# Kernel optimization log

Measured on AMD Instinct MI355X. Metric: run time of the kernel, lower is better.

## Reference

```python
import jax, jax.numpy as jnp
import numpy as np


def setup_inputs() -> dict:
    key = jax.random.key(0)
    ks = jax.random.split(key, 9)
    B, Q, K, F, C = 16, 2048, 2048, 128, 2
    q = jax.random.normal(ks[0], (B, Q, F), dtype=jnp.float32)
    k = jax.random.normal(ks[1], (B, K, F), dtype=jnp.float32)
    v = jax.random.normal(ks[2], (B, K, F), dtype=jnp.float32)
    coords_q = jax.random.uniform(ks[3], (B, Q, C), dtype=jnp.float32)
    coords_k = jax.random.uniform(ks[4], (B, K, C), dtype=jnp.float32)
    attn_mask = jax.random.randint(ks[5], (B, Q, K), 0, 2).astype(jnp.bool_)
    alibi_mask = jax.random.randint(ks[6], (B, Q, K), 0, 2).astype(jnp.bool_)
    bias_scale = jax.random.uniform(ks[7], (1,), dtype=jnp.float32)  # nn.Parameter(torch.rand(1))
    running_mean = jnp.ones((1,), dtype=jnp.float32)  # RunningMeanScaler buffer (eval mode)
    return {"q": q, "k": k, "v": v, "coords_q": coords_q, "coords_k": coords_k,
            "attn_mask": attn_mask, "alibi_mask": alibi_mask,
            "bias_scale": bias_scale, "running_mean": running_mean}


def reference(q, k, v, coords_q, coords_k, attn_mask, alibi_mask, bias_scale, running_mean):
    # [b,q,k] attention logits
    scale = jnp.asarray(k.shape[-1], q.dtype) ** -0.5
    weight_logits = jnp.einsum('bqf,bkf->bqk', q, k) * scale
    # pairwise coordinate distances [b,q,k]
    diff = coords_q[:, :, None, :] - coords_k[:, None, :, :]
    distances = jnp.sqrt(jnp.sum(diff * diff, axis=-1))
    scaled_distances = (distances / running_mean) * bias_scale  # broadcast scalars
    masked_distances = jnp.where(alibi_mask, jnp.zeros((), distances.dtype), scaled_distances)
    weights = jax.nn.softmax(weight_logits, axis=-1)
    masked = jnp.where(attn_mask, jnp.zeros((), weights.dtype), weights - masked_distances)
    attention = jnp.einsum('bqk,bkf->bqf', masked, v)
    return attention
```

## Files before the change

### kernel.cpp

```cpp
#include <hip/hip_runtime.h>
#include <stdint.h>

#define B_  16
#define QL  2048
#define KL  2048
#define FD  128
#define BQ  64
#define BK  32

typedef __attribute__((ext_vector_type(8))) short bf16x8;
typedef __attribute__((ext_vector_type(4))) float f32x4;

__device__ __forceinline__ unsigned short f2b(float f) {
  union { float f; unsigned u; } x; x.f = f;
  unsigned r = x.u + 0x7fffu + ((x.u >> 16) & 1u);
  return (unsigned short)(r >> 16);
}

__global__ __launch_bounds__(256, 2) void alibi_attn(
    const float* __restrict__ qp,
    const float* __restrict__ kp,
    const float* __restrict__ vp,
    const float* __restrict__ cqp,
    const float* __restrict__ ckp,
    const int* __restrict__ amp,
    const int* __restrict__ almp,
    const float* __restrict__ bsp,
    const float* __restrict__ rmp,
    float* __restrict__ outp)
{
  __shared__ unsigned short kv[8192];
  __shared__ unsigned short plds[4][2][16 * 40];

  const int t    = threadIdx.x;
  const int w    = t >> 6;
  const int lane = t & 63;
  const int l15  = lane & 15;
  const int q4   = lane >> 4;

  const int bid  = blockIdx.x;
  const int xcd  = bid & 7, slot = bid >> 3;
  const int b    = (xcd << 1) | (slot >> 5);
  const int qt   = slot & 31;
  const int qbase = qt * BQ;

  const float bscale = bsp[0] / rmp[0];
  const float scale  = 0.08838834764831845f;

  {
    const float* qg = qp + ((long long)(b * QL + qbase)) * FD;
    #pragma unroll
    for (int i = 0; i < 8; ++i) {
      float4 u = ((const float4*)qg)[t + 256 * i];
      ushort4 s4;
      s4.x = f2b(u.x); s4.y = f2b(u.y); s4.z = f2b(u.z); s4.w = f2b(u.w);
      *(ushort4*)&kv[(t + 256 * i) * 4] = s4;
    }
  }
  __syncthreads();
  bf16x8 qfrag[4];
  {
    const int m = w * 16 + l15;
    #pragma unroll
    for (int fs = 0; fs < 4; ++fs)
      qfrag[fs] = *(const bf16x8*)&kv[m * 128 + fs * 32 + q4 * 8];
  }
  float cqx[4], cqy[4];
  #pragma unroll
  for (int r = 0; r < 4; ++r) {
    const int qg_ = qbase + w * 16 + q4 * 4 + r;
    cqx[r] = cqp[((long long)(b * QL + qg_)) * 2 + 0];
    cqy[r] = cqp[((long long)(b * QL + qg_)) * 2 + 1];
  }
  __syncthreads();

  f32x4 O1[8], O2[8];
  #pragma unroll
  for (int n = 0; n < 8; ++n) {
    O1[n] = (f32x4){0.f, 0.f, 0.f, 0.f};
    O2[n] = (f32x4){0.f, 0.f, 0.f, 0.f};
  }
  float lsum[4] = {0.f, 0.f, 0.f, 0.f};

  const int kr_st = t >> 3;
  const int fb_st = (t & 7) * 16;
  const float* kg_base = kp + ((long long)b * KL) * FD;
  const float* vg_base = vp + ((long long)b * KL) * FD;

  for (int kt = 0; kt < KL / BK; ++kt) {
    const int k0 = kt * BK;

    float4 kld[4], vld[4];
    #pragma unroll
    for (int i = 0; i < 4; ++i) {
      kld[i] = *(const float4*)(kg_base + (long long)(k0 + kr_st) * FD + fb_st + 4 * i);
      vld[i] = *(const float4*)(vg_base + (long long)(k0 + kr_st) * FD + fb_st + 4 * i);
    }
    int am_[2][4], al_[2][4];
    float ckx_[2], cky_[2];
    #pragma unroll
    for (int s = 0; s < 2; ++s) {
      const int kg = k0 + s * 16 + l15;
      #pragma unroll
      for (int r = 0; r < 4; ++r) {
        const int qg_ = qbase + w * 16 + q4 * 4 + r;
        const long long mi = ((long long)(b * QL + qg_)) * KL + kg;
        am_[s][r] = __builtin_nontemporal_load(amp + mi);
        al_[s][r] = __builtin_nontemporal_load(almp + mi);
      }
      float2 c2 = *(const float2*)(ckp + ((long long)(b * KL + kg)) * 2);
      ckx_[s] = c2.x; cky_[s] = c2.y;
    }

    __syncthreads();
    #pragma unroll
    for (int i = 0; i < 4; ++i) {
      ushort4 s4;
      s4.x = f2b(kld[i].x); s4.y = f2b(kld[i].y);
      s4.z = f2b(kld[i].z); s4.w = f2b(kld[i].w);
      *(ushort4*)&kv[kr_st * 128 + fb_st + 4 * i] = s4;
      const int f0 = fb_st + 4 * i;
      kv[4096 + (f0 + 0) * 32 + kr_st] = f2b(vld[i].x);
      kv[4096 + (f0 + 1) * 32 + kr_st] = f2b(vld[i].y);
      kv[4096 + (f0 + 2) * 32 + kr_st] = f2b(vld[i].z);
      kv[4096 + (f0 + 3) * 32 + kr_st] = f2b(vld[i].w);
    }
    __syncthreads();

    f32x4 S0 = (f32x4){0.f, 0.f, 0.f, 0.f};
    f32x4 S1 = (f32x4){0.f, 0.f, 0.f, 0.f};
    #pragma unroll
    for (int fs = 0; fs < 4; ++fs) {
      bf16x8 kb0 = *(const bf16x8*)&kv[(l15)      * 128 + fs * 32 + q4 * 8];
      bf16x8 kb1 = *(const bf16x8*)&kv[(16 + l15) * 128 + fs * 32 + q4 * 8];
      S0 = __builtin_amdgcn_mfma_f32_16x16x32_bf16(qfrag[fs], kb0, S0, 0, 0, 0);
      S1 = __builtin_amdgcn_mfma_f32_16x16x32_bf16(qfrag[fs], kb1, S1, 0, 0, 0);
    }

    #pragma unroll
    for (int s = 0; s < 2; ++s) {
      const f32x4 Sv = s ? S1 : S0;
      #pragma unroll
      for (int r = 0; r < 4; ++r) {
        float e = __expf(Sv[r] * scale);
        lsum[r] += e;
        float dx = cqx[r] - ckx_[s], dy = cqy[r] - cky_[s];
        float d  = sqrtf(fmaf(dx, dx, dy * dy)) * bscale;
        float wv = am_[s][r] ? 0.f : e;
        float tv = (am_[s][r] | al_[s][r]) ? 0.f : d;
        const int m = q4 * 4 + r, c = s * 16 + l15;
        plds[w][0][m * 40 + c] = f2b(wv);
        plds[w][1][m * 40 + c] = f2b(tv);
      }
    }
    __syncthreads();

    bf16x8 aw = *(const bf16x8*)&plds[w][0][l15 * 40 + q4 * 8];
    bf16x8 at = *(const bf16x8*)&plds[w][1][l15 * 40 + q4 * 8];
    #pragma unroll
    for (int n = 0; n < 8; ++n) {
      bf16x8 vb = *(const bf16x8*)&kv[4096 + (n * 16 + l15) * 32 + q4 * 8];
      O1[n] = __builtin_amdgcn_mfma_f32_16x16x32_bf16(aw, vb, O1[n], 0, 0, 0);
      O2[n] = __builtin_amdgcn_mfma_f32_16x16x32_bf16(at, vb, O2[n], 0, 0, 0);
    }
  }

  #pragma unroll
  for (int off = 1; off < 16; off <<= 1) {
    #pragma unroll
    for (int r = 0; r < 4; ++r) lsum[r] += __shfl_xor(lsum[r], off, 64);
  }
  float linv[4];
  #pragma unroll
  for (int r = 0; r < 4; ++r) linv[r] = 1.0f / lsum[r];

  #pragma unroll
  for (int n = 0; n < 8; ++n) {
    #pragma unroll
    for (int r = 0; r < 4; ++r) {
      const int qg_ = qbase + w * 16 + q4 * 4 + r;
      const int f   = n * 16 + l15;
      float val = O1[n][r] * linv[r] - O2[n][r];
      __builtin_nontemporal_store(val, outp + ((long long)(b * QL + qg_)) * FD + f);
    }
  }
}

extern "C" void kernel_launch(void* const* d_in, const int* in_sizes, int n_in,
                              void* d_out, int out_size, void* d_ws, size_t ws_size,
                              hipStream_t stream) {
  const float* q   = (const float*)d_in[0];
  const float* k   = (const float*)d_in[1];
  const float* v   = (const float*)d_in[2];
  const float* cq  = (const float*)d_in[3];
  const float* ck  = (const float*)d_in[4];
  const int*   am  = (const int*)d_in[5];
  const int*   alm = (const int*)d_in[6];
  const float* bs  = (const float*)d_in[7];
  const float* rm  = (const float*)d_in[8];
  float*       out = (float*)d_out;

  dim3 grid(B_ * (QL / BQ));
  dim3 block(256);
  hipLaunchKernelGGL(alibi_attn, grid, block, 0, stream,
                     q, k, v, cq, ck, am, alm, bs, rm, out);
}
```

Before: 751.9 us.

## Double-buffer K/V tiles in LDS with register prefetch and padded strides

Splits the K/V LDS staging into two buffers so the global loads (K, V, masks, coordinates) for the next tile are issued before the current tile's MFMAs, then converted and stored into the other buffer. This cuts the per-step barriers from three to one. It also pads the LDS row strides to reduce bank conflicts, switches exp to exp2 with a folded scale, and uses cheaper round-half-up bf16 conversion. The costs are doubled LDS and more registers, which may threaten two blocks per CU, plus slightly different rounding.

```diff
diff --git a/kernel.cpp b/kernel.cpp
--- a/kernel.cpp
+++ b/kernel.cpp
@@ -7,14 +7,20 @@
 #define FD  128
 #define BQ  64
 #define BK  32
+#define NSTEP (KL/BK)
+
+#define KSTR  136
+#define VTOFF 4352
+#define VTSTR 40
+#define BUFSHORTS 9472
+#define PSTR  40
 
 typedef __attribute__((ext_vector_type(8))) short bf16x8;
 typedef __attribute__((ext_vector_type(4))) float f32x4;
 
 __device__ __forceinline__ unsigned short f2b(float f) {
   union { float f; unsigned u; } x; x.f = f;
-  unsigned r = x.u + 0x7fffu + ((x.u >> 16) & 1u);
-  return (unsigned short)(r >> 16);
+  return (unsigned short)((x.u + 0x8000u) >> 16);
 }
 
 __global__ __launch_bounds__(256, 2) void alibi_attn(
@@ -29,8 +35,8 @@
     const float* __restrict__ rmp,
     float* __restrict__ outp)
 {
-  __shared__ unsigned short kv[8192];
-  __shared__ unsigned short plds[4][2][16 * 40];
+  __shared__ unsigned short kv[2 * BUFSHORTS];
+  __shared__ unsigned short plds[4][2][16 * PSTR];
 
   const int t    = threadIdx.x;
   const int w    = t >> 6;
@@ -41,20 +47,23 @@
   const int bid  = blockIdx.x;
   const int xcd  = bid & 7, slot = bid >> 3;
   const int b    = (xcd << 1) | (slot >> 5);
-  const int qt   = slot & 31;
-  const int qbase = qt * BQ;
+  const int qbase = (slot & 31) * BQ;
 
   const float bscale = bsp[0] / rmp[0];
-  const float scale  = 0.08838834764831845f;
+  const float sl2 = 0.08838834764831845f * 1.44269504089f;
+
+  const int kr_st = t >> 3;
+  const int fb_st = (t & 7) * 4;
 
   {
     const float* qg = qp + ((long long)(b * QL + qbase)) * FD;
     #pragma unroll
     for (int i = 0; i < 8; ++i) {
-      float4 u = ((const float4*)qg)[t + 256 * i];
-      ushort4 s4;
-      s4.x = f2b(u.x); s4.y = f2b(u.y); s4.z = f2b(u.z); s4.w = f2b(u.w);
-      *(ushort4*)&kv[(t + 256 * i) * 4] = s4;
+      int idx = t + 256 * i;
+      float4 u = ((const float4*)qg)[idx];
+      int row = idx >> 5, col = (idx & 31) * 4;
+      ushort4 s4; s4.x = f2b(u.x); s4.y = f2b(u.y); s4.z = f2b(u.z); s4.w = f2b(u.w);
+      *(ushort4*)&kv[row * KSTR + col] = s4;
     }
   }
   __syncthreads();
@@ -63,14 +72,53 @@
     const int m = w * 16 + l15;
     #pragma unroll
     for (int fs = 0; fs < 4; ++fs)
-      qfrag[fs] = *(const bf16x8*)&kv[m * 128 + fs * 32 + q4 * 8];
+      qfrag[fs] = *(const bf16x8*)&kv[m * KSTR + fs * 32 + q4 * 8];
   }
   float cqx[4], cqy[4];
+  long long mrow_base[4];
   #pragma unroll
   for (int r = 0; r < 4; ++r) {
     const int qg_ = qbase + w * 16 + q4 * 4 + r;
-    cqx[r] = cqp[((long long)(b * QL + qg_)) * 2 + 0];
-    cqy[r] = cqp[((long long)(b * QL + qg_)) * 2 + 1];
+    float2 c2 = *(const float2*)(cqp + ((long long)(b * QL + qg_)) * 2);
+    cqx[r] = c2.x; cqy[r] = c2.y;
+    mrow_base[r] = ((long long)(b * QL + qg_)) * KL;
+  }
+  __syncthreads();
+
+  const float* kgb = kp + ((long long)b * KL) * FD;
+  const float* vgb = vp + ((long long)b * KL) * FD;
+
+  int am_b[2][2][4], al_b[2][2][4];
+  float ckx_b[2][2], cky_b[2][2];
+  #pragma unroll
+  for (int s = 0; s < 2; ++s) {
+    const int kg = s * 16 + l15;
+    #pragma unroll
+    for (int r = 0; r < 4; ++r) {
+      am_b[0][s][r] = __builtin_nontemporal_load(amp + mrow_base[r] + kg);
+      al_b[0][s][r] = __builtin_nontemporal_load(almp + mrow_base[r] + kg);
+    }
+    float2 c2 = *(const float2*)(ckp + ((long long)(b * KL + kg)) * 2);
+    ckx_b[0][s] = c2.x; cky_b[0][s] = c2.y;
+  }
+  {
+    float4 kld[4], vld[4];
+    #pragma unroll
+    for (int i = 0; i < 4; ++i) {
+      kld[i] = *(const float4*)(kgb + (long long)kr_st * FD + fb_st + 32 * i);
+      vld[i] = *(const float4*)(vgb + (long long)kr_st * FD + fb_st + 32 * i);
+    }
+    #pragma unroll
+    for (int i = 0; i < 4; ++i) {
+      ushort4 s4; s4.x = f2b(kld[i].x); s4.y = f2b(kld[i].y);
+      s4.z = f2b(kld[i].z); s4.w = f2b(kld[i].w);
+      *(ushort4*)&kv[kr_st * KSTR + fb_st + 32 * i] = s4;
+      const int f0 = fb_st + 32 * i;
+      kv[VTOFF + (f0 + 0) * VTSTR + kr_st] = f2b(vld[i].x);
+      kv[VTOFF + (f0 + 1) * VTSTR + kr_st] = f2b(vld[i].y);
+      kv[VTOFF + (f0 + 2) * VTSTR + kr_st] = f2b(vld[i].z);
+      kv[VTOFF + (f0 + 3) * VTSTR + kr_st] = f2b(vld[i].w);
+    }
   }
   __syncthreads();
 
@@ -82,57 +130,38 @@
   }
   float lsum[4] = {0.f, 0.f, 0.f, 0.f};
 
-  const int kr_st = t >> 3;
-  const int fb_st = (t & 7) * 16;
-  const float* kg_base = kp + ((long long)b * KL) * FD;
-  const float* vg_base = vp + ((long long)b * KL) * FD;
-
-  for (int kt = 0; kt < KL / BK; ++kt) {
-    const int k0 = kt * BK;
+  #pragma unroll 2
+  for (int kt = 0; kt < NSTEP; ++kt) {
+    const int cur = kt & 1, nxt = cur ^ 1;
+    const unsigned short* kb = kv + cur * BUFSHORTS;
+    unsigned short*       nb = kv + nxt * BUFSHORTS;
+    const int ktp = (kt + 1 < NSTEP) ? (kt + 1) : kt;
+    const int k0p = ktp * BK;
 
     float4 kld[4], vld[4];
     #pragma unroll
     for (int i = 0; i < 4; ++i) {
-      kld[i] = *(const float4*)(kg_base + (long long)(k0 + kr_st) * FD + fb_st + 4 * i);
-      vld[i] = *(const float4*)(vg_base + (long long)(k0 + kr_st) * FD + fb_st + 4 * i);
-    }
-    int am_[2][4], al_[2][4];
-    float ckx_[2], cky_[2];
+      kld[i] = *(const float4*)(kgb + (long long)(k0p + kr_st) * FD + fb_st + 32 * i);
+      vld[i] = *(const float4*)(vgb + (long long)(k0p + kr_st) * FD + fb_st + 32 * i);
+    }
     #pragma unroll
     for (int s = 0; s < 2; ++s) {
-      const int kg = k0 + s * 16 + l15;
+      const int kg = k0p + s * 16 + l15;
       #pragma unroll
       for (int r = 0; r < 4; ++r) {
-        const int qg_ = qbase + w * 16 + q4 * 4 + r;
-        const long long mi = ((long long)(b * QL + qg_)) * KL + kg;
-        am_[s][r] = __builtin_nontemporal_load(amp + mi);
-        al_[s][r] = __builtin_nontemporal_load(almp + mi);
+        am_b[nxt][s][r] = __builtin_nontemporal_load(amp + mrow_base[r] + kg);
+        al_b[nxt][s][r] = __builtin_nontemporal_load(almp + mrow_base[r] + kg);
       }
       float2 c2 = *(const float2*)(ckp + ((long long)(b * KL + kg)) * 2);
-      ckx_[s] = c2.x; cky_[s] = c2.y;
-    }
-
-    __syncthreads();
-    #pragma unroll
-    for (int i = 0; i < 4; ++i) {
-      ushort4 s4;
-      s4.x = f2b(kld[i].x); s4.y = f2b(kld[i].y);
-      s4.z = f2b(kld[i].z); s4.w = f2b(kld[i].w);
-      *(ushort4*)&kv[kr_st * 128 + fb_st + 4 * i] = s4;
-      const int f0 = fb_st + 4 * i;
-      kv[4096 + (f0 + 0) * 32 + kr_st] = f2b(vld[i].x);
-      kv[4096 + (f0 + 1) * 32 + kr_st] = f2b(vld[i].y);
-      kv[4096 + (f0 + 2) * 32 + kr_st] = f2b(vld[i].z);
-      kv[4096 + (f0 + 3) * 32 + kr_st] = f2b(vld[i].w);
-    }
-    __syncthreads();
+      ckx_b[nxt][s] = c2.x; cky_b[nxt][s] = c2.y;
+    }
 
     f32x4 S0 = (f32x4){0.f, 0.f, 0.f, 0.f};
     f32x4 S1 = (f32x4){0.f, 0.f, 0.f, 0.f};
     #pragma unroll
     for (int fs = 0; fs < 4; ++fs) {
-      bf16x8 kb0 = *(const bf16x8*)&kv[(l15)      * 128 + fs * 32 + q4 * 8];
-      bf16x8 kb1 = *(const bf16x8*)&kv[(16 + l15) * 128 + fs * 32 + q4 * 8];
+      bf16x8 kb0 = *(const bf16x8*)&kb[(l15)      * KSTR + fs * 32 + q4 * 8];
+      bf16x8 kb1 = *(const bf16x8*)&kb[(16 + l15) * KSTR + fs * 32 + q4 * 8];
       S0 = __builtin_amdgcn_mfma_f32_16x16x32_bf16(qfrag[fs], kb0, S0, 0, 0, 0);
       S1 = __builtin_amdgcn_mfma_f32_16x16x32_bf16(qfrag[fs], kb1, S1, 0, 0, 0);
     }
@@ -142,27 +171,40 @@
       const f32x4 Sv = s ? S1 : S0;
       #pragma unroll
       for (int r = 0; r < 4; ++r) {
-        float e = __expf(Sv[r] * scale);
+        float e = __builtin_amdgcn_exp2f(Sv[r] * sl2);
         lsum[r] += e;
-        float dx = cqx[r] - ckx_[s], dy = cqy[r] - cky_[s];
+        float dx = cqx[r] - ckx_b[cur][s], dy = cqy[r] - cky_b[cur][s];
         float d  = sqrtf(fmaf(dx, dx, dy * dy)) * bscale;
-        float wv = am_[s][r] ? 0.f : e;
-        float tv = (am_[s][r] | al_[s][r]) ? 0.f : d;
-        const int m = q4 * 4 + r, c = s * 16 + l15;
-        plds[w][0][m * 40 + c] = f2b(wv);
-        plds[w][1][m * 40 + c] = f2b(tv);
+        int am = am_b[cur][s][r], al = al_b[cur][s][r];
+        float wv = am ? 0.f : e;
+        float tv = (am | al) ? 0.f : d;
+        const int mm = q4 * 4 + r, c = s * 16 + l15;
+        plds[w][0][mm * PSTR + c] = f2b(wv);
+        plds[w][1][mm * PSTR + c] = f2b(tv);
       }
     }
-    __syncthreads();
-
-    bf16x8 aw = *(const bf16x8*)&plds[w][0][l15 * 40 + q4 * 8];
-    bf16x8 at = *(const bf16x8*)&plds[w][1][l15 * 40 + q4 * 8];
+
+    bf16x8 aw = *(const bf16x8*)&plds[w][0][l15 * PSTR + q4 * 8];
+    bf16x8 at = *(const bf16x8*)&plds[w][1][l15 * PSTR + q4 * 8];
     #pragma unroll
     for (int n = 0; n < 8; ++n) {
-      bf16x8 vb = *(const bf16x8*)&kv[4096 + (n * 16 + l15) * 32 + q4 * 8];
+      bf16x8 vb = *(const bf16x8*)&kb[VTOFF + (n * 16 + l15) * VTSTR + q4 * 8];
       O1[n] = __builtin_amdgcn_mfma_f32_16x16x32_bf16(aw, vb, O1[n], 0, 0, 0);
       O2[n] = __builtin_amdgcn_mfma_f32_16x16x32_bf16(at, vb, O2[n], 0, 0, 0);
     }
+
+    #pragma unroll
+    for (int i = 0; i < 4; ++i) {
+      ushort4 s4; s4.x = f2b(kld[i].x); s4.y = f2b(kld[i].y);
+      s4.z = f2b(kld[i].z); s4.w = f2b(kld[i].w);
+      *(ushort4*)&nb[kr_st * KSTR + fb_st + 32 * i] = s4;
+      const int f0 = fb_st + 32 * i;
+      nb[VTOFF + (f0 + 0) * VTSTR + kr_st] = f2b(vld[i].x);
+      nb[VTOFF + (f0 + 1) * VTSTR + kr_st] = f2b(vld[i].y);
+      nb[VTOFF + (f0 + 2) * VTSTR + kr_st] = f2b(vld[i].z);
+      nb[VTOFF + (f0 + 3) * VTSTR + kr_st] = f2b(vld[i].w);
+    }
+    __syncthreads();
   }
 
   #pragma unroll
```

Measured after the change: 676.2 us. 10.1% less time.
